# Performance work log

Hardware: AMD Instinct MI355X
Metric: run time of the kernel (lower is better)

The kernel has to match this reference:

```python
import jax, jax.numpy as jnp
import numpy as np

NUM_HEADS = 8
LOGIT_MAX = float(np.log(1.0 / 0.01))  # log(100)


def setup_inputs() -> dict:
    key = jax.random.key(0)
    kq, kk, kv, kp = jax.random.split(key, 4)
    B, n, L, C = 16, 100, 64, 256
    return {
        "query": jax.random.normal(kq, (B, n, L, C), dtype=jnp.float32),
        "key": jax.random.normal(kk, (B, n, L, C), dtype=jnp.float32),
        "value": jax.random.normal(kv, (B, n, L, C), dtype=jnp.float32),
        "position": jax.random.normal(kp, (B, NUM_HEADS, L, L), dtype=jnp.float32),
        "logit_scale": jnp.full((NUM_HEADS, 1, 1), np.log(10.0), dtype=jnp.float32),
    }


def reference(query, key, value, position, logit_scale):
    B, n, Lq, C = query.shape
    Lv = key.shape[2]
    H = NUM_HEADS
    Dh = C // H
    q = query.reshape(B, n, Lq, H, Dh)
    k = key.reshape(B, n, Lv, H, Dh)
    v = value.reshape(B, n, Lv, H, Dh)
    # [B, n, H, Lq, Lv]
    attn = jnp.einsum("bnqhd,bnkhd->bnhqk", q, k)
    scale = jnp.exp(jnp.minimum(logit_scale, LOGIT_MAX))  # (H,1,1)
    attn = attn * scale + position[:, None]  # broadcast over window dim n
    attn = jax.nn.softmax(attn, axis=-1)
    x = jnp.einsum("bnhqk,bnkhd->bnqhd", attn, v).reshape(B, n, Lq, C)
    return (x, attn)
```

## Files before the change

### kernel.cpp

```cpp
#include <hip/hip_runtime.h>


typedef __attribute__((ext_vector_type(8))) short bf16x8;
typedef __attribute__((ext_vector_type(4))) float f32x4;

#define LOGIT_MAX_F 4.605170185988091f

__device__ __forceinline__ short f2bf(float f) {
    union { float f; unsigned u; } c; c.f = f;
    unsigned r = c.u + 0x7FFFu + ((c.u >> 16) & 1u);
    return (short)(r >> 16);
}
__device__ __forceinline__ float bf2f(short s) {
    union { unsigned u; float f; } c; c.u = ((unsigned)(unsigned short)s) << 16;
    return c.f;
}

#define QHI_OFF 0
#define QLO_OFF 2560
#define KHI_OFF 5120
#define KLO_OFF 7680
#define VT_OFF  10240
#define P_OFF   0
#define SMEM_SHORTS 12544

__global__ __launch_bounds__(256, 5) void tat_attn_kernel(
    const float* __restrict__ Qg, const float* __restrict__ Kg,
    const float* __restrict__ Vg, const float* __restrict__ Pg,
    const float* __restrict__ LSg,
    float* __restrict__ Xout, float* __restrict__ Aout)
{
    constexpr int L = 64, C = 256, H = 8, NW = 100;
    __shared__ short smem[SMEM_SHORTS];

    const int blk = blockIdx.x;
    const int h  = blk & 7;
    const int bw = blk >> 3;
    const int t  = threadIdx.x;
    const int wave = t >> 6;
    const int lane = t & 63;
    const int quad = lane >> 4;
    const int l15  = lane & 15;

    const float* qb = Qg + (size_t)bw * L * C + h * 32;
    const float* kb = Kg + (size_t)bw * L * C + h * 32;
    const float* vb = Vg + (size_t)bw * L * C + h * 32;
    const int b = bw / NW;
    const float* pb = Pg + (size_t)(b * H + h) * L * L;
    float* xb = Xout + (size_t)bw * L * C + h * 32;
    float* ab = Aout + ((size_t)bw * H + h) * L * L;

    const float scale = __expf(fminf(LSg[h], LOGIT_MAX_F));

    {
        const int r8 = t >> 2;
        const int c8 = (t & 3) * 8;
        const float4 q0 = *(const float4*)(qb + r8 * C + c8);
        const float4 q1 = *(const float4*)(qb + r8 * C + c8 + 4);
        const float4 k0 = *(const float4*)(kb + r8 * C + c8);
        const float4 k1 = *(const float4*)(kb + r8 * C + c8 + 4);
        const float qa[8] = {q0.x,q0.y,q0.z,q0.w,q1.x,q1.y,q1.z,q1.w};
        const float ka[8] = {k0.x,k0.y,k0.z,k0.w,k1.x,k1.y,k1.z,k1.w};
        bf16x8 qh, ql, kh, kl;
        #pragma unroll
        for (int i = 0; i < 8; ++i) {
            const short qhi = f2bf(qa[i]);
            qh[i] = qhi; ql[i] = f2bf(qa[i] - bf2f(qhi));
            const short khi = f2bf(ka[i]);
            kh[i] = khi; kl[i] = f2bf(ka[i] - bf2f(khi));
        }
        *(bf16x8*)(smem + QHI_OFF + r8 * 40 + c8) = qh;
        *(bf16x8*)(smem + QLO_OFF + r8 * 40 + c8) = ql;
        *(bf16x8*)(smem + KHI_OFF + r8 * 40 + c8) = kh;
        *(bf16x8*)(smem + KLO_OFF + r8 * 40 + c8) = kl;

        const int kk = t & 63;
        const int db = (t >> 6) * 8;
        const float4 v0 = *(const float4*)(vb + kk * C + db);
        const float4 v1 = *(const float4*)(vb + kk * C + db + 4);
        const float va[8] = {v0.x,v0.y,v0.z,v0.w,v1.x,v1.y,v1.z,v1.w};
        #pragma unroll
        for (int i = 0; i < 8; ++i)
            smem[VT_OFF + (db + i) * 72 + kk] = f2bf(va[i]);
    }
    __syncthreads();

    f32x4 acc0 = {0,0,0,0}, acc1 = {0,0,0,0}, acc2 = {0,0,0,0}, acc3 = {0,0,0,0};
    {
        const bf16x8 aqh = *(const bf16x8*)(smem + QHI_OFF + (16*wave + l15)*40 + quad*8);
        const bf16x8 aql = *(const bf16x8*)(smem + QLO_OFF + (16*wave + l15)*40 + quad*8);
        #pragma unroll
        for (int t4 = 0; t4 < 4; ++t4) {
            const bf16x8 bkh = *(const bf16x8*)(smem + KHI_OFF + (16*t4 + l15)*40 + quad*8);
            const bf16x8 bkl = *(const bf16x8*)(smem + KLO_OFF + (16*t4 + l15)*40 + quad*8);
            f32x4 a = (t4==0)?acc0:(t4==1)?acc1:(t4==2)?acc2:acc3;
            a = __builtin_amdgcn_mfma_f32_16x16x32_bf16(aqh, bkh, a, 0, 0, 0);
            a = __builtin_amdgcn_mfma_f32_16x16x32_bf16(aqh, bkl, a, 0, 0, 0);
            a = __builtin_amdgcn_mfma_f32_16x16x32_bf16(aql, bkh, a, 0, 0, 0);
            if (t4==0) acc0 = a; else if (t4==1) acc1 = a; else if (t4==2) acc2 = a; else acc3 = a;
        }
    }

    float lg[4][4];
    #pragma unroll
    for (int r = 0; r < 4; ++r) {
        const int row = 16*wave + quad*4 + r;
        const int cb  = row * L + l15;
        lg[0][r] = fmaf(acc0[r], scale, pb[cb + 0]);
        lg[1][r] = fmaf(acc1[r], scale, pb[cb + 16]);
        lg[2][r] = fmaf(acc2[r], scale, pb[cb + 32]);
        lg[3][r] = fmaf(acc3[r], scale, pb[cb + 48]);
    }

    float p[4][4];
    #pragma unroll
    for (int r = 0; r < 4; ++r) {
        float m = fmaxf(fmaxf(lg[0][r], lg[1][r]), fmaxf(lg[2][r], lg[3][r]));
        #pragma unroll
        for (int off = 8; off > 0; off >>= 1) m = fmaxf(m, __shfl_xor(m, off));
        const float e0 = __expf(lg[0][r] - m);
        const float e1 = __expf(lg[1][r] - m);
        const float e2 = __expf(lg[2][r] - m);
        const float e3 = __expf(lg[3][r] - m);
        float s = (e0 + e1) + (e2 + e3);
        #pragma unroll
        for (int off = 8; off > 0; off >>= 1) s += __shfl_xor(s, off);
        const float inv = 1.0f / s;
        p[0][r] = e0 * inv; p[1][r] = e1 * inv; p[2][r] = e2 * inv; p[3][r] = e3 * inv;
    }

    __syncthreads();

    #pragma unroll
    for (int r = 0; r < 4; ++r) {
        const int row = 16*wave + quad*4 + r;
        #pragma unroll
        for (int t4 = 0; t4 < 4; ++t4) {
            const int col = 16*t4 + l15;
            ab[row * L + col] = p[t4][r];
            smem[P_OFF + row * 72 + col] = f2bf(p[t4][r]);
        }
    }

    f32x4 o0 = {0,0,0,0}, o1 = {0,0,0,0};
    #pragma unroll
    for (int hh = 0; hh < 2; ++hh) {
        const bf16x8 ap = *(const bf16x8*)(smem + P_OFF + (16*wave + l15)*72 + hh*32 + quad*8);
        const bf16x8 bv0 = *(const bf16x8*)(smem + VT_OFF + l15*72        + hh*32 + quad*8);
        const bf16x8 bv1 = *(const bf16x8*)(smem + VT_OFF + (l15+16)*72   + hh*32 + quad*8);
        o0 = __builtin_amdgcn_mfma_f32_16x16x32_bf16(ap, bv0, o0, 0, 0, 0);
        o1 = __builtin_amdgcn_mfma_f32_16x16x32_bf16(ap, bv1, o1, 0, 0, 0);
    }

    #pragma unroll
    for (int r = 0; r < 4; ++r) {
        const int row = 16*wave + quad*4 + r;
        xb[row * C + l15]      = o0[r];
        xb[row * C + 16 + l15] = o1[r];
    }
}

extern "C" void kernel_launch(void* const* d_in, const int* in_sizes, int n_in,
                              void* d_out, int out_size, void* d_ws, size_t ws_size,
                              hipStream_t stream) {
    const float* q   = (const float*)d_in[0];
    const float* k   = (const float*)d_in[1];
    const float* v   = (const float*)d_in[2];
    const float* pos = (const float*)d_in[3];
    const float* ls  = (const float*)d_in[4];
    float* out = (float*)d_out;

    constexpr int B = 16, NW = 100, L = 64, C = 256, H = 8;
    float* x_out = out;
    float* a_out = out + (size_t)B * NW * L * C;

    const int blocks = B * NW * H;
    tat_attn_kernel<<<blocks, 256, 0, stream>>>(q, k, v, pos, ls, x_out, a_out);
}
```

Measured before the change: 539.4 us.

## Load Q/K fragments directly from global into registers, drop LDS staging

```diff
diff --git a/kernel.cpp b/kernel.cpp
--- a/kernel.cpp
+++ b/kernel.cpp
@@ -16,13 +16,27 @@
     return c.f;
 }
 
-#define QHI_OFF 0
-#define QLO_OFF 2560
-#define KHI_OFF 5120
-#define KLO_OFF 7680
-#define VT_OFF  10240
-#define P_OFF   0
-#define SMEM_SHORTS 12544
+#define VT_OFF 0
+#define P_OFF  (32 * 72)
+#define SMEM_SHORTS (32 * 72 + 64 * 72)
+
+__device__ __forceinline__ f32x4 qk_tile(const float4 ka, const float4 kb2,
+                                         const bf16x8 qh, const bf16x8 ql,
+                                         f32x4 acc)
+{
+    const float kf[8] = {ka.x, ka.y, ka.z, ka.w, kb2.x, kb2.y, kb2.z, kb2.w};
+    bf16x8 kh, kl;
+    #pragma unroll
+    for (int i = 0; i < 8; ++i) {
+        const short hi = f2bf(kf[i]);
+        kh[i] = hi;
+        kl[i] = f2bf(kf[i] - bf2f(hi));
+    }
+    acc = __builtin_amdgcn_mfma_f32_16x16x32_bf16(qh, kh, acc, 0, 0, 0);
+    acc = __builtin_amdgcn_mfma_f32_16x16x32_bf16(qh, kl, acc, 0, 0, 0);
+    acc = __builtin_amdgcn_mfma_f32_16x16x32_bf16(ql, kh, acc, 0, 0, 0);
+    return acc;
+}
 
 __global__ __launch_bounds__(256, 5) void tat_attn_kernel(
     const float* __restrict__ Qg, const float* __restrict__ Kg,
@@ -52,59 +66,49 @@
 
     const float scale = __expf(fminf(LSg[h], LOGIT_MAX_F));
 
+    const float4 v0 = *(const float4*)(vb + lane * C + wave * 8);
+    const float4 v1 = *(const float4*)(vb + lane * C + wave * 8 + 4);
+    const int qrow = 16 * wave + l15;
+    const float4 q0 = *(const float4*)(qb + qrow * C + quad * 8);
+    const float4 q1 = *(const float4*)(qb + qrow * C + quad * 8 + 4);
+    const float4 k0a = *(const float4*)(kb + l15 * C + quad * 8);
+    const float4 k0b = *(const float4*)(kb + l15 * C + quad * 8 + 4);
+    const float4 k1a = *(const float4*)(kb + (16 + l15) * C + quad * 8);
+    const float4 k1b = *(const float4*)(kb + (16 + l15) * C + quad * 8 + 4);
+
     {
-        const int r8 = t >> 2;
-        const int c8 = (t & 3) * 8;
-        const float4 q0 = *(const float4*)(qb + r8 * C + c8);
-        const float4 q1 = *(const float4*)(qb + r8 * C + c8 + 4);
-        const float4 k0 = *(const float4*)(kb + r8 * C + c8);
-        const float4 k1 = *(const float4*)(kb + r8 * C + c8 + 4);
-        const float qa[8] = {q0.x,q0.y,q0.z,q0.w,q1.x,q1.y,q1.z,q1.w};
-        const float ka[8] = {k0.x,k0.y,k0.z,k0.w,k1.x,k1.y,k1.z,k1.w};
-        bf16x8 qh, ql, kh, kl;
+        const float va[8] = {v0.x, v0.y, v0.z, v0.w, v1.x, v1.y, v1.z, v1.w};
+        #pragma unroll
+        for (int i = 0; i < 8; ++i)
+            smem[VT_OFF + (wave * 8 + i) * 72 + lane] = f2bf(va[i]);
+    }
+
+    bf16x8 qh, ql;
+    {
+        const float qa[8] = {q0.x, q0.y, q0.z, q0.w, q1.x, q1.y, q1.z, q1.w};
         #pragma unroll
         for (int i = 0; i < 8; ++i) {
-            const short qhi = f2bf(qa[i]);
-            qh[i] = qhi; ql[i] = f2bf(qa[i] - bf2f(qhi));
-            const short khi = f2bf(ka[i]);
-            kh[i] = khi; kl[i] = f2bf(ka[i] - bf2f(khi));
+            const short hi = f2bf(qa[i]);
+            qh[i] = hi;
+            ql[i] = f2bf(qa[i] - bf2f(hi));
         }
-        *(bf16x8*)(smem + QHI_OFF + r8 * 40 + c8) = qh;
-        *(bf16x8*)(smem + QLO_OFF + r8 * 40 + c8) = ql;
-        *(bf16x8*)(smem + KHI_OFF + r8 * 40 + c8) = kh;
-        *(bf16x8*)(smem + KLO_OFF + r8 * 40 + c8) = kl;
+    }
 
-        const int kk = t & 63;
-        const int db = (t >> 6) * 8;
-        const float4 v0 = *(const float4*)(vb + kk * C + db);
-        const float4 v1 = *(const float4*)(vb + kk * C + db + 4);
-        const float va[8] = {v0.x,v0.y,v0.z,v0.w,v1.x,v1.y,v1.z,v1.w};
-        #pragma unroll
-        for (int i = 0; i < 8; ++i)
-            smem[VT_OFF + (db + i) * 72 + kk] = f2bf(va[i]);
-    }
-    __syncthreads();
+    const float4 k2a = *(const float4*)(kb + (32 + l15) * C + quad * 8);
+    const float4 k2b = *(const float4*)(kb + (32 + l15) * C + quad * 8 + 4);
+    const float4 k3a = *(const float4*)(kb + (48 + l15) * C + quad * 8);
+    const float4 k3b = *(const float4*)(kb + (48 + l15) * C + quad * 8 + 4);
 
     f32x4 acc0 = {0,0,0,0}, acc1 = {0,0,0,0}, acc2 = {0,0,0,0}, acc3 = {0,0,0,0};
-    {
-        const bf16x8 aqh = *(const bf16x8*)(smem + QHI_OFF + (16*wave + l15)*40 + quad*8);
-        const bf16x8 aql = *(const bf16x8*)(smem + QLO_OFF + (16*wave + l15)*40 + quad*8);
-        #pragma unroll
-        for (int t4 = 0; t4 < 4; ++t4) {
-            const bf16x8 bkh = *(const bf16x8*)(smem + KHI_OFF + (16*t4 + l15)*40 + quad*8);
-            const bf16x8 bkl = *(const bf16x8*)(smem + KLO_OFF + (16*t4 + l15)*40 + quad*8);
-            f32x4 a = (t4==0)?acc0:(t4==1)?acc1:(t4==2)?acc2:acc3;
-            a = __builtin_amdgcn_mfma_f32_16x16x32_bf16(aqh, bkh, a, 0, 0, 0);
-            a = __builtin_amdgcn_mfma_f32_16x16x32_bf16(aqh, bkl, a, 0, 0, 0);
-            a = __builtin_amdgcn_mfma_f32_16x16x32_bf16(aql, bkh, a, 0, 0, 0);
-            if (t4==0) acc0 = a; else if (t4==1) acc1 = a; else if (t4==2) acc2 = a; else acc3 = a;
-        }
-    }
+    acc0 = qk_tile(k0a, k0b, qh, ql, acc0);
+    acc1 = qk_tile(k1a, k1b, qh, ql, acc1);
+    acc2 = qk_tile(k2a, k2b, qh, ql, acc2);
+    acc3 = qk_tile(k3a, k3b, qh, ql, acc3);
 
     float lg[4][4];
     #pragma unroll
     for (int r = 0; r < 4; ++r) {
-        const int row = 16*wave + quad*4 + r;
+        const int row = 16 * wave + quad * 4 + r;
         const int cb  = row * L + l15;
         lg[0][r] = fmaf(acc0[r], scale, pb[cb + 0]);
         lg[1][r] = fmaf(acc1[r], scale, pb[cb + 16]);
@@ -129,32 +133,32 @@
         p[0][r] = e0 * inv; p[1][r] = e1 * inv; p[2][r] = e2 * inv; p[3][r] = e3 * inv;
     }
 
-    __syncthreads();
-
     #pragma unroll
     for (int r = 0; r < 4; ++r) {
-        const int row = 16*wave + quad*4 + r;
+        const int row = 16 * wave + quad * 4 + r;
         #pragma unroll
         for (int t4 = 0; t4 < 4; ++t4) {
-            const int col = 16*t4 + l15;
+            const int col = 16 * t4 + l15;
             ab[row * L + col] = p[t4][r];
             smem[P_OFF + row * 72 + col] = f2bf(p[t4][r]);
         }
     }
 
+    __syncthreads();
+
     f32x4 o0 = {0,0,0,0}, o1 = {0,0,0,0};
     #pragma unroll
     for (int hh = 0; hh < 2; ++hh) {
-        const bf16x8 ap = *(const bf16x8*)(smem + P_OFF + (16*wave + l15)*72 + hh*32 + quad*8);
-        const bf16x8 bv0 = *(const bf16x8*)(smem + VT_OFF + l15*72        + hh*32 + quad*8);
-        const bf16x8 bv1 = *(const bf16x8*)(smem + VT_OFF + (l15+16)*72   + hh*32 + quad*8);
+        const bf16x8 ap  = *(const bf16x8*)(smem + P_OFF + (16 * wave + l15) * 72 + hh * 32 + quad * 8);
+        const bf16x8 bv0 = *(const bf16x8*)(smem + VT_OFF + l15 * 72        + hh * 32 + quad * 8);
+        const bf16x8 bv1 = *(const bf16x8*)(smem + VT_OFF + (l15 + 16) * 72 + hh * 32 + quad * 8);
         o0 = __builtin_amdgcn_mfma_f32_16x16x32_bf16(ap, bv0, o0, 0, 0, 0);
         o1 = __builtin_amdgcn_mfma_f32_16x16x32_bf16(ap, bv1, o1, 0, 0, 0);
     }
 
     #pragma unroll
     for (int r = 0; r < 4; ++r) {
-        const int row = 16*wave + quad*4 + r;
+        const int row = 16 * wave + quad * 4 + r;
         xb[row * C + l15]      = o0[r];
         xb[row * C + 16 + l15] = o1[r];
     }
```

Measured after the change: 583.8 us. 1.08x slower.
